# Kernel optimization log

Measured on AMD Instinct MI355X. Metric: run time of the kernel, lower is better.

Reference implementation:

```python
import jax, jax.numpy as jnp
import numpy as np

B, N, K, D, A, V = 2, 32768, 16, 256, 64, 64


def setup_inputs() -> dict:
    key = jax.random.key(0)
    ks = jax.random.split(key, 20)
    r = lambda i, shape: jax.random.normal(ks[i], shape, jnp.float32) * 0.02
    return dict(
        x=jax.random.normal(ks[0], (B, N, D), jnp.float32),
        knn_idx=jax.random.randint(ks[1], (N, K), 0, N),
        knn_rel_pos=jax.random.normal(ks[2], (N, K, 3), jnp.float32),
        g1=jnp.ones((D,), jnp.float32), b1=jnp.zeros((D,), jnp.float32),
        g2=jnp.ones((D,), jnp.float32), b2=jnp.zeros((D,), jnp.float32),
        Wq=r(3, (D, A)), bq=jnp.zeros((A,), jnp.float32),
        Wk=r(4, (D, A)), bk=jnp.zeros((A,), jnp.float32),
        Wv=r(5, (D, V)), bv=jnp.zeros((V,), jnp.float32),
        Wo=r(6, (V, D)), bo=jnp.zeros((D,), jnp.float32),
        Wpa1=r(7, (3, A)), bpa1=jnp.zeros((A,), jnp.float32),
        Wpa2=r(8, (A, A)), bpa2=jnp.zeros((A,), jnp.float32),
        Wpv1=r(9, (3, V)), bpv1=jnp.zeros((V,), jnp.float32),
        Wpv2=r(10, (V, V)), bpv2=jnp.zeros((V,), jnp.float32),
        Ws1=r(11, (A, A)), bs1=jnp.zeros((A,), jnp.float32),
        Ws2=r(12, (A, 1)), bs2=jnp.zeros((1,), jnp.float32),
        Wf1=r(13, (D, 2 * D)), bf1=jnpp if False else jnp.zeros((2 * D,), jnp.float32),
        Wf2=r(14, (2 * D, D)), bf2=jnp.zeros((D,), jnp.float32),
    )


def _ln(t, g, b):
    m = t.mean(-1, keepdims=True)
    var = ((t - m) ** 2).mean(-1, keepdims=True)
    return (t - m) * jax.lax.rsqrt(var + 1e-5) * g + b


def reference(x, knn_idx, knn_rel_pos, g1, b1, g2, b2,
              Wq, bq, Wk, bk, Wv, bv, Wo, bo,
              Wpa1, bpa1, Wpa2, bpa2, Wpv1, bpv1, Wpv2, bpv2,
              Ws1, bs1, Ws2, bs2, Wf1, bf1, Wf2, bf2):
    scale = jnp.sqrt(jnp.float32(A))
    h = _ln(x, g1, b1)                       # [B,N,D]
    q = h @ Wq + bq                          # [B,N,A]
    k_all = h @ Wk + bk                      # [B,N,A]
    v_all = h @ Wv + bv                      # [B,N,V]
    kn = k_all[:, knn_idx]                   # gather -> [B,N,K,A]
    vn = v_all[:, knn_idx]                   # [B,N,K,V]
    ra = jax.nn.relu(knn_rel_pos @ Wpa1 + bpa1) @ Wpa2 + bpa2  # [N,K,A]
    rv = jax.nn.relu(knn_rel_pos @ Wpv1 + bpv1) @ Wpv2 + bpv2  # [N,K,V]
    t = jnp.tanh(q[:, :, None, :] - kn + ra[None])             # [B,N,K,A]
    score = (jax.nn.relu(t @ Ws1 + bs1) @ Ws2 + bs2)[..., 0]   # [B,N,K]
    attn = jax.nn.softmax(score / scale, axis=2)
    ctx = jnp.einsum('bnk,bnkv->bnv', attn, vn + rv[None])     # [B,N,V]
    x = x + ctx @ Wo + bo
    h2 = _ln(x, g2, b2)
    x = x + (jax.nn.gelu(h2 @ Wf1 + bf1, approximate=False) @ Wf2 + bf2)
    return x
```

## Files before the change

kernel.cpp:

```cpp
#include <hip/hip_runtime.h>
#include <hip/hip_bf16.h>
#include <math.h>

#define BB 2
#define NN 32768
#define KK 16
#define DD 256
#define AA 64
#define VV 64

typedef __attribute__((ext_vector_type(8))) short bf16x8;
typedef __attribute__((ext_vector_type(4))) float f32x4;
typedef __attribute__((ext_vector_type(4))) unsigned short u16x4;

__device__ __forceinline__ ushort f2bf(float v) {
  __hip_bfloat16 b = __float2bfloat16(v);
  ushort u; __builtin_memcpy(&u, &b, 2);
  return u;
}

__device__ __forceinline__ void astore(ushort* A, int row, int col, float v) {
  int off = (row * 128 + col * 2) ^ ((row & 7) << 4);
  *reinterpret_cast<ushort*>(reinterpret_cast<char*>(A) + off) = f2bf(v);
}
__device__ __forceinline__ void zstore8(ushort* A, int row, int chunk) {
  int off = (row * 128 + chunk * 8) ^ ((row & 7) << 4);
  *reinterpret_cast<unsigned long long*>(reinterpret_cast<char*>(A) + off) = 0ULL;
}
__device__ __forceinline__ bf16x8 afrag(const ushort* A, int rowbase, int lane, int ks) {
  int row = rowbase + (lane & 15), g = lane >> 4;
  int off = (row * 128 + ks * 64 + g * 16) ^ ((row & 7) << 4);
  return *reinterpret_cast<const bf16x8*>(reinterpret_cast<const char*>(A) + off);
}
__device__ __forceinline__ bf16x8 loadfrag(const ushort* p, int fi, int lane) {
  return *reinterpret_cast<const bf16x8*>(&p[((size_t)fi * 64 + lane) * 8]);
}

__global__ __launch_bounds__(256) void k_prep(
    const float* __restrict__ Wq, const float* __restrict__ Wk, const float* __restrict__ Wv,
    const float* __restrict__ Wf1, const float* __restrict__ Wf2,
    const float* __restrict__ Wpa2, const float* __restrict__ Wpv2,
    const float* __restrict__ Ws1, const float* __restrict__ Wo,
    ushort* __restrict__ pQKV, ushort* __restrict__ pWf1, ushort* __restrict__ pWf2,
    ushort* __restrict__ pS, ushort* __restrict__ pWo) {
  int tid = blockIdx.x * 256 + threadIdx.x;
  int lane = tid & 63, g = lane >> 4, c16 = lane & 15;
  bf16x8 f;
  if (tid < 6144) {
    int fi = tid >> 6; int ks = fi / 12, nt = fi % 12;
    int col = nt * 16 + c16;
    const float* W = (col < 64) ? Wq : (col < 128) ? Wk : Wv;
    int c = col & 63;
#pragma unroll
    for (int e = 0; e < 8; e++) f[e] = (short)f2bf(W[(ks * 32 + g * 8 + e) * 64 + c]);
    *reinterpret_cast<bf16x8*>(&pQKV[(size_t)tid * 8]) = f;
  } else if (tid < 22528) {
    int t2 = tid - 6144; int fi = t2 >> 6; int ks = fi >> 5, nt = fi & 31;
    int col = nt * 16 + c16;
#pragma unroll
    for (int e = 0; e < 8; e++) f[e] = (short)f2bf(Wf1[(ks * 32 + g * 8 + e) * 512 + col]);
    *reinterpret_cast<bf16x8*>(&pWf1[(size_t)t2 * 8]) = f;
  } else if (tid < 38912) {
    int t3 = tid - 22528; int fi = t3 >> 6; int ks = fi >> 4, nt = fi & 15;
    int col = nt * 16 + c16;
#pragma unroll
    for (int e = 0; e < 8; e++) f[e] = (short)f2bf(Wf2[(ks * 32 + g * 8 + e) * 256 + col]);
    *reinterpret_cast<bf16x8*>(&pWf2[(size_t)t3 * 8]) = f;
  } else if (tid < 40448) {
    int t4 = tid - 38912; int fi = t4 >> 6;
    int mat = fi >> 3, ks = (fi >> 2) & 1, nt = fi & 3;
    const float* W = (mat == 0) ? Wpa2 : (mat == 1) ? Wpv2 : Ws1;
    int col = nt * 16 + c16;
#pragma unroll
    for (int e = 0; e < 8; e++) f[e] = (short)f2bf(W[(ks * 32 + g * 8 + e) * 64 + col]);
    *reinterpret_cast<bf16x8*>(&pS[(size_t)t4 * 8]) = f;
  } else if (tid < 42496) {
    int t5 = tid - 40448; int fi = t5 >> 6; int ks = fi >> 4, nt = fi & 15;
    int col = nt * 16 + c16;
#pragma unroll
    for (int e = 0; e < 8; e++) f[e] = (short)f2bf(Wo[(ks * 32 + g * 8 + e) * 256 + col]);
    *reinterpret_cast<bf16x8*>(&pWo[(size_t)t5 * 8]) = f;
  }
}

__global__ __launch_bounds__(256) void k_qkv(
    const float* __restrict__ x, const float* __restrict__ g1, const float* __restrict__ b1,
    const ushort* __restrict__ pW,
    const float* __restrict__ bq, const float* __restrict__ bk, const float* __restrict__ bv,
    float* __restrict__ qo, float* __restrict__ ko, float* __restrict__ vo) {
  __shared__ __align__(16) ushort hs[32 * 256];
  int t = threadIdx.x, lane = t & 63, w = t >> 6;
  size_t row0 = (size_t)blockIdx.x * 32;

  {
    const float4 gv = *reinterpret_cast<const float4*>(&g1[lane * 4]);
    const float4 bvv = *reinterpret_cast<const float4*>(&b1[lane * 4]);
#pragma unroll
    for (int r8 = 0; r8 < 8; r8++) {
      int r = w * 8 + r8;
      const float4 xv = *reinterpret_cast<const float4*>(&x[(row0 + r) * DD + lane * 4]);
      float s = xv.x + xv.y + xv.z + xv.w;
      float s2 = xv.x * xv.x + xv.y * xv.y + xv.z * xv.z + xv.w * xv.w;
      for (int o = 32; o > 0; o >>= 1) { s += __shfl_down(s, o, 64); s2 += __shfl_down(s2, o, 64); }
      s = __shfl(s, 0, 64); s2 = __shfl(s2, 0, 64);
      float m = s * (1.f / DD), rs = rsqrtf(s2 * (1.f / DD) - m * m + 1e-5f);
      u16x4 hv;
      hv[0] = f2bf((xv.x - m) * rs * gv.x + bvv.x);
      hv[1] = f2bf((xv.y - m) * rs * gv.y + bvv.y);
      hv[2] = f2bf((xv.z - m) * rs * gv.z + bvv.z);
      hv[3] = f2bf((xv.w - m) * rs * gv.w + bvv.w);
      int off = (r * 512 + lane * 8) ^ ((r & 7) << 4);
      *reinterpret_cast<u16x4*>(reinterpret_cast<char*>(hs) + off) = hv;
    }
  }
  __syncthreads();

  f32x4 acc[2][3] = {};
  for (int ks = 0; ks < 8; ks++) {
    int rowa = lane & 15, g = lane >> 4;
    bf16x8 a0 = *reinterpret_cast<const bf16x8*>(reinterpret_cast<const char*>(hs) +
                 ((rowa * 512 + ks * 64 + g * 16) ^ ((rowa & 7) << 4)));
    int rowb = rowa + 16;
    bf16x8 a1 = *reinterpret_cast<const bf16x8*>(reinterpret_cast<const char*>(hs) +
                 ((rowb * 512 + ks * 64 + g * 16) ^ ((rowb & 7) << 4)));
#pragma unroll
    for (int j = 0; j < 3; j++) {
      int fi = ks * 12 + w * 3 + j;
      bf16x8 bw = *reinterpret_cast<const bf16x8*>(&pW[((size_t)fi * 64 + lane) * 8]);
      acc[0][j] = __builtin_amdgcn_mfma_f32_16x16x32_bf16(a0, bw, acc[0][j], 0, 0, 0);
      acc[1][j] = __builtin_amdgcn_mfma_f32_16x16x32_bf16(a1, bw, acc[1][j], 0, 0, 0);
    }
  }

#pragma unroll
  for (int j = 0; j < 3; j++) {
    int ntg = w * 3 + j;
    int buf = ntg >> 2;
    float* out = (buf == 0) ? qo : (buf == 1) ? ko : vo;
    const float* bias = (buf == 0) ? bq : (buf == 1) ? bk : bv;
    int col = (ntg & 3) * 16 + (lane & 15);
    float bb = bias[col];
#pragma unroll
    for (int mt = 0; mt < 2; mt++)
#pragma unroll
      for (int r = 0; r < 4; r++) {
        int row = mt * 16 + (lane >> 4) * 4 + r;
        out[(row0 + row) * 64 + col] = acc[mt][j][r] + bb;
      }
  }
}

__global__ __launch_bounds__(256) void k_attn(
    const float* __restrict__ x, const float* __restrict__ relpos, const int* __restrict__ knn,
    const float* __restrict__ qg, const float* __restrict__ kg, const float* __restrict__ vg,
    const float* __restrict__ Wpa1, const float* __restrict__ bpa1, const float* __restrict__ bpa2,
    const float* __restrict__ Wpv1, const float* __restrict__ bpv1, const float* __restrict__ bpv2,
    const ushort* __restrict__ pS, const float* __restrict__ bs1,
    const float* __restrict__ Ws2, const float* __restrict__ bs2,
    const ushort* __restrict__ pWo, const float* __restrict__ bo,
    float* __restrict__ xmid) {
  int n0 = blockIdx.x * 2;
  int t = threadIdx.x, lane = t & 63, w = t >> 6;
  int g = lane >> 4, c16 = lane & 15;

  __shared__ __align__(16) ushort A0[64 * 64];
  __shared__ float ra_ls[32][64];
  __shared__ float rv_ls[32][64];
  __shared__ __align__(16) ushort ctile[16 * 64];
  __shared__ float qv[4][64];
  __shared__ float scp[64][4];
  __shared__ float attn_s[64];
  __shared__ float rp_s[2][48];
  __shared__ int idx_s[2][16];

  if (t < 32) idx_s[t >> 4][t & 15] = knn[(n0 + (t >> 4)) * KK + (t & 15)];
  if (t >= 64 && t < 160) {
    int i = t - 64;
    rp_s[i / 48][i % 48] = relpos[(size_t)n0 * 48 + i];
  }
  if (t >= 160 && t < 160 + 192) {
    int i = t - 160;
    zstore8(ctile, 4 + (i >> 4), i & 15);
  }
  qv[w][lane] = qg[((size_t)(w & 1) * NN + n0 + (w >> 1)) * AA + lane];
  __syncthreads();

  {
    const float* W1 = (w < 2) ? Wpa1 : Wpv1;
    const float* bb1 = (w < 2) ? bpa1 : bpv1;
    float wa0 = W1[lane], wa1 = W1[64 + lane], wa2 = W1[128 + lane], ba = bb1[lane];
    int pt = w & 1;
#pragma unroll
    for (int j = 0; j < 16; j++) {
      float r0 = rp_s[pt][j * 3], r1 = rp_s[pt][j * 3 + 1], r2 = rp_s[pt][j * 3 + 2];
      float v = fmaxf(ba + r0 * wa0 + r1 * wa1 + r2 * wa2, 0.f);
      astore(A0, w * 16 + j, lane, v);
    }
  }
  __syncthreads();

  {
    bf16x8 bwa0 = loadfrag(pS, 0 + 0 + w, lane);
    bf16x8 bwa1 = loadfrag(pS, 0 + 4 + w, lane);
    bf16x8 bwv0 = loadfrag(pS, 8 + 0 + w, lane);
    bf16x8 bwv1 = loadfrag(pS, 8 + 4 + w, lane);
    int col = w * 16 + c16;
    float ba2 = bpa2[col], bv2 = bpv2[col];
#pragma unroll
    for (int mt = 0; mt < 2; mt++) {
      bf16x8 a0 = afrag(A0, mt * 16, lane, 0), a1 = afrag(A0, mt * 16, lane, 1);
      f32x4 acc = {0.f, 0.f, 0.f, 0.f};
      acc = __builtin_amdgcn_mfma_f32_16x16x32_bf16(a0, bwa0, acc, 0, 0, 0);
      acc = __builtin_amdgcn_mfma_f32_16x16x32_bf16(a1, bwa1, acc, 0, 0, 0);
#pragma unroll
      for (int r = 0; r < 4; r++) ra_ls[mt * 16 + g * 4 + r][col] = acc[r] + ba2;
      bf16x8 v0 = afrag(A0, 32 + mt * 16, lane, 0), v1 = afrag(A0, 32 + mt * 16, lane, 1);
      f32x4 accv = {0.f, 0.f, 0.f, 0.f};
      accv = __builtin_amdgcn_mfma_f32_16x16x32_bf16(v0, bwv0, accv, 0, 0, 0);
      accv = __builtin_amdgcn_mfma_f32_16x16x32_bf16(v1, bwv1, accv, 0, 0, 0);
#pragma unroll
      for (int r = 0; r < 4; r++) rv_ls[mt * 16 + g * 4 + r][col] = accv[r] + bv2;
    }
  }
  __syncthreads();

  {
    int pt = w >> 1, b = w & 1;
    float qq = qv[w][lane];
#pragma unroll
    for (int k = 0; k < 16; k++) {
      float kvv = kg[((size_t)b * NN + idx_s[pt][k]) * AA + lane];
      float xx = qq - kvv + ra_ls[pt * 16 + k][lane];
      float ex = __expf(2.f * xx);
      float tv = 1.f - 2.f * __builtin_amdgcn_rcpf(ex + 1.f);
      astore(A0, w * 16 + k, lane, tv);
    }
  }
  __syncthreads();

  {
    bf16x8 fsA = loadfrag(pS, 16 + 0 + w, lane);
    bf16x8 fsB = loadfrag(pS, 16 + 4 + w, lane);
    int col = w * 16 + c16;
    float bsc = bs1[col], wsc = Ws2[col];
    f32x4 pp[4];
#pragma unroll
    for (int mt = 0; mt < 4; mt++) {
      bf16x8 a0 = afrag(A0, mt * 16, lane, 0), a1 = afrag(A0, mt * 16, lane, 1);
      f32x4 acc = {0.f, 0.f, 0.f, 0.f};
      acc = __builtin_amdgcn_mfma_f32_16x16x32_bf16(a0, fsA, acc, 0, 0, 0);
      acc = __builtin_amdgcn_mfma_f32_16x16x32_bf16(a1, fsB, acc, 0, 0, 0);
#pragma unroll
      for (int r = 0; r < 4; r++) acc[r] = fmaxf(acc[r] + bsc, 0.f) * wsc;
      pp[mt] = acc;
    }
#pragma unroll
    for (int o = 1; o < 16; o <<= 1)
#pragma unroll
      for (int mt = 0; mt < 4; mt++)
#pragma unroll
        for (int r = 0; r < 4; r++) pp[mt][r] += __shfl_xor(pp[mt][r], o, 64);
    if (c16 == 0)
#pragma unroll
      for (int mt = 0; mt < 4; mt++)
#pragma unroll
        for (int r = 0; r < 4; r++) scp[mt * 16 + g * 4 + r][w] = pp[mt][r];
  }
  __syncthreads();

  if (t < 64) {
    float4 s4 = *reinterpret_cast<const float4*>(&scp[t][0]);
    float sc = (s4.x + s4.y + s4.z + s4.w + bs2[0]) * 0.125f;
    float mx = sc;
#pragma unroll
    for (int o = 8; o > 0; o >>= 1) mx = fmaxf(mx, __shfl_xor(mx, o, 64));
    float e = __expf(sc - mx);
    float ss = e;
#pragma unroll
    for (int o = 8; o > 0; o >>= 1) ss += __shfl_xor(ss, o, 64);
    attn_s[t] = e / ss;
  }
  __syncthreads();

  {
    int pt = w >> 1, b = w & 1;
    float acc = 0.f;
#pragma unroll
    for (int k = 0; k < 16; k++) {
      float vn = vg[((size_t)b * NN + idx_s[pt][k]) * VV + lane] + rv_ls[pt * 16 + k][lane];
      acc += attn_s[w * 16 + k] * vn;
    }
    astore(ctile, w, lane, acc);
  }
  __syncthreads();

  {
    bf16x8 a0 = afrag(ctile, 0, lane, 0), a1 = afrag(ctile, 0, lane, 1);
    f32x4 acc[4];
#pragma unroll
    for (int j = 0; j < 4; j++) {
      bf16x8 b0 = loadfrag(pWo, 0 + w * 4 + j, lane);
      bf16x8 b1 = loadfrag(pWo, 16 + w * 4 + j, lane);
      f32x4 a = {0.f, 0.f, 0.f, 0.f};
      a = __builtin_amdgcn_mfma_f32_16x16x32_bf16(a0, b0, a, 0, 0, 0);
      a = __builtin_amdgcn_mfma_f32_16x16x32_bf16(a1, b1, a, 0, 0, 0);
      acc[j] = a;
    }
    if (g == 0) {
#pragma unroll
      for (int j = 0; j < 4; j++) {
        int col = w * 64 + j * 16 + c16;
        float bb = bo[col];
#pragma unroll
        for (int r = 0; r < 4; r++) {
          int pt = r >> 1, b = r & 1;
          size_t addr = ((size_t)b * NN + n0 + pt) * DD + col;
          xmid[addr] = x[addr] + acc[j][r] + bb;
        }
      }
    }
  }
}

__global__ __launch_bounds__(256) void k_ffn(
    const float* __restrict__ xmid, const float* __restrict__ g2, const float* __restrict__ b2,
    const ushort* __restrict__ pWf1, const float* __restrict__ bf1,
    const ushort* __restrict__ pWf2, const float* __restrict__ bf2,
    float* __restrict__ out) {
  __shared__ __align__(16) ushort hs[32 * 256];
  __shared__ __align__(16) ushort ys[32 * 512];
  int t = threadIdx.x, lane = t & 63, w = t >> 6;
  size_t row0 = (size_t)blockIdx.x * 32;

  {
    const float4 gv = *reinterpret_cast<const float4*>(&g2[lane * 4]);
    const float4 bvv = *reinterpret_cast<const float4*>(&b2[lane * 4]);
#pragma unroll
    for (int r8 = 0; r8 < 8; r8++) {
      int r = w * 8 + r8;
      const float4 xv = *reinterpret_cast<const float4*>(&xmid[(row0 + r) * DD + lane * 4]);
      float s = xv.x + xv.y + xv.z + xv.w;
      float s2 = xv.x * xv.x + xv.y * xv.y + xv.z * xv.z + xv.w * xv.w;
      for (int o = 32; o > 0; o >>= 1) { s += __shfl_down(s, o, 64); s2 += __shfl_down(s2, o, 64); }
      s = __shfl(s, 0, 64); s2 = __shfl(s2, 0, 64);
      float m = s * (1.f / DD), rs = rsqrtf(s2 * (1.f / DD) - m * m + 1e-5f);
      u16x4 hv;
      hv[0] = f2bf((xv.x - m) * rs * gv.x + bvv.x);
      hv[1] = f2bf((xv.y - m) * rs * gv.y + bvv.y);
      hv[2] = f2bf((xv.z - m) * rs * gv.z + bvv.z);
      hv[3] = f2bf((xv.w - m) * rs * gv.w + bvv.w);
      int off = (r * 512 + lane * 8) ^ ((r & 7) << 4);
      *reinterpret_cast<u16x4*>(reinterpret_cast<char*>(hs) + off) = hv;
    }
  }
  __syncthreads();

  f32x4 acc1[2][8] = {};
  for (int ks = 0; ks < 8; ks++) {
    int rowa = lane & 15, g = lane >> 4;
    bf16x8 a0 = *reinterpret_cast<const bf16x8*>(reinterpret_cast<const char*>(hs) +
                 ((rowa * 512 + ks * 64 + g * 16) ^ ((rowa & 7) << 4)));
    int rowb = rowa + 16;
    bf16x8 a1 = *reinterpret_cast<const bf16x8*>(reinterpret_cast<const char*>(hs) +
                 ((rowb * 512 + ks * 64 + g * 16) ^ ((rowb & 7) << 4)));
#pragma unroll
    for (int j = 0; j < 8; j++) {
      int fi = ks * 32 + w * 8 + j;
      bf16x8 bw = *reinterpret_cast<const bf16x8*>(&pWf1[((size_t)fi * 64 + lane) * 8]);
      acc1[0][j] = __builtin_amdgcn_mfma_f32_16x16x32_bf16(a0, bw, acc1[0][j], 0, 0, 0);
      acc1[1][j] = __builtin_amdgcn_mfma_f32_16x16x32_bf16(a1, bw, acc1[1][j], 0, 0, 0);
    }
  }

#pragma unroll
  for (int j = 0; j < 8; j++) {
    int col = w * 128 + j * 16 + (lane & 15);
    float bb = bf1[col];
#pragma unroll
    for (int mt = 0; mt < 2; mt++)
#pragma unroll
      for (int r = 0; r < 4; r++) {
        float v = acc1[mt][j][r] + bb;
        v = v * 0.5f * (1.f + erff(v * 0.70710678118654752f));
        int row = mt * 16 + (lane >> 4) * 4 + r;
        int off = (row * 1024 + col * 2) ^ ((row & 7) << 4);
        *reinterpret_cast<ushort*>(reinterpret_cast<char*>(ys) + off) = f2bf(v);
      }
  }
  __syncthreads();

  f32x4 acc2[2][4] = {};
  for (int ks = 0; ks < 16; ks++) {
    int rowa = lane & 15, g = lane >> 4;
    bf16x8 a0 = *reinterpret_cast<const bf16x8*>(reinterpret_cast<const char*>(ys) +
                 ((rowa * 1024 + ks * 64 + g * 16) ^ ((rowa & 7) << 4)));
    int rowb = rowa + 16;
    bf16x8 a1 = *reinterpret_cast<const bf16x8*>(reinterpret_cast<const char*>(ys) +
                 ((rowb * 1024 + ks * 64 + g * 16) ^ ((rowb & 7) << 4)));
#pragma unroll
    for (int j = 0; j < 4; j++) {
      int fi = ks * 16 + w * 4 + j;
      bf16x8 bw = *reinterpret_cast<const bf16x8*>(&pWf2[((size_t)fi * 64 + lane) * 8]);
      acc2[0][j] = __builtin_amdgcn_mfma_f32_16x16x32_bf16(a0, bw, acc2[0][j], 0, 0, 0);
      acc2[1][j] = __builtin_amdgcn_mfma_f32_16x16x32_bf16(a1, bw, acc2[1][j], 0, 0, 0);
    }
  }

#pragma unroll
  for (int j = 0; j < 4; j++) {
    int col = w * 64 + j * 16 + (lane & 15);
    float bb = bf2[col];
#pragma unroll
    for (int mt = 0; mt < 2; mt++)
#pragma unroll
      for (int r = 0; r < 4; r++) {
        int row = mt * 16 + (lane >> 4) * 4 + r;
        size_t idx = (row0 + row) * DD + col;
        out[idx] = xmid[idx] + acc2[mt][j][r] + bb;
      }
  }
}

extern "C" void kernel_launch(void* const* d_in, const int* in_sizes, int n_in,
                              void* d_out, int out_size, void* d_ws, size_t ws_size,
                              hipStream_t stream) {
  const float* x      = (const float*)d_in[0];
  const int*   knn    = (const int*)  d_in[1];
  const float* relpos = (const float*)d_in[2];
  const float* g1     = (const float*)d_in[3];
  const float* b1     = (const float*)d_in[4];
  const float* g2     = (const float*)d_in[5];
  const float* b2     = (const float*)d_in[6];
  const float* Wq     = (const float*)d_in[7];
  const float* bq     = (const float*)d_in[8];
  const float* Wk     = (const float*)d_in[9];
  const float* bk     = (const float*)d_in[10];
  const float* Wv     = (const float*)d_in[11];
  const float* bv     = (const float*)d_in[12];
  const float* Wo     = (const float*)d_in[13];
  const float* bo     = (const float*)d_in[14];
  const float* Wpa1   = (const float*)d_in[15];
  const float* bpa1   = (const float*)d_in[16];
  const float* Wpa2   = (const float*)d_in[17];
  const float* bpa2   = (const float*)d_in[18];
  const float* Wpv1   = (const float*)d_in[19];
  const float* bpv1   = (const float*)d_in[20];
  const float* Wpv2   = (const float*)d_in[21];
  const float* bpv2   = (const float*)d_in[22];
  const float* Ws1    = (const float*)d_in[23];
  const float* bs1    = (const float*)d_in[24];
  const float* Ws2    = (const float*)d_in[25];
  const float* bs2    = (const float*)d_in[26];
  const float* Wf1    = (const float*)d_in[27];
  const float* bf1    = (const float*)d_in[28];
  const float* Wf2    = (const float*)d_in[29];
  const float* bf2    = (const float*)d_in[30];

  float* ws   = (float*)d_ws;
  float* q    = ws;
  float* kk   = q  + (size_t)BB * NN * AA;
  float* vv   = kk + (size_t)BB * NN * AA;
  float* xmid = vv + (size_t)BB * NN * VV;
  ushort* pQKV = (ushort*)(xmid + (size_t)BB * NN * DD);
  ushort* pWf1 = pQKV + 49152;
  ushort* pWf2 = pWf1 + 131072;
  ushort* pS   = pWf2 + 131072;
  ushort* pWo  = pS + 12288;

  k_prep<<<166, 256, 0, stream>>>(Wq, Wk, Wv, Wf1, Wf2, Wpa2, Wpv2, Ws1, Wo,
                                  pQKV, pWf1, pWf2, pS, pWo);
  k_qkv<<<(BB * NN) / 32, 256, 0, stream>>>(x, g1, b1, pQKV, bq, bk, bv, q, kk, vv);
  k_attn<<<NN / 2, 256, 0, stream>>>(x, relpos, knn, q, kk, vv,
                                     Wpa1, bpa1, bpa2, Wpv1, bpv1, bpv2,
                                     pS, bs1, Ws2, bs2, pWo, bo, xmid);
  k_ffn<<<(BB * NN) / 32, 256, 0, stream>>>(xmid, g2, b2, pWf1, bf1, pWf2, bf2, (float*)d_out);
}
```

Baseline: 474.2 us.

## Store q/k/v and positional encodings in bf16 with paired-column processing

q, k and v intermediates are written as bf16 instead of fp32, which halves global traffic for the neighbour gathers in the attention kernel. The ra/rv tables in shared memory become bf16, and the tanh and weighted-sum loops now handle two columns per lane across half the neighbours, with a cross-half shuffle reduction. The score reduction swaps per-lane shuffles for a shared-memory partial buffer summed by 64 threads. Precision drops for q/k/v and the positional terms, and the larger shared-memory footprint may reduce occupancy.

```diff
diff --git a/kernel.cpp b/kernel.cpp
--- a/kernel.cpp
+++ b/kernel.cpp
@@ -18,10 +18,13 @@
   ushort u; __builtin_memcpy(&u, &b, 2);
   return u;
 }
-
-__device__ __forceinline__ void astore(ushort* A, int row, int col, float v) {
-  int off = (row * 128 + col * 2) ^ ((row & 7) << 4);
-  *reinterpret_cast<ushort*>(reinterpret_cast<char*>(A) + off) = f2bf(v);
+__device__ __forceinline__ float bflo(unsigned u) { return __uint_as_float(u << 16); }
+__device__ __forceinline__ float bfhi(unsigned u) { return __uint_as_float(u & 0xffff0000u); }
+
+__device__ __forceinline__ void astore2(ushort* A, int row, int colpair, float lo, float hi) {
+  int off = (row * 128 + colpair * 4) ^ ((row & 7) << 4);
+  unsigned u = ((unsigned)f2bf(hi) << 16) | (unsigned)f2bf(lo);
+  *reinterpret_cast<unsigned*>(reinterpret_cast<char*>(A) + off) = u;
 }
 __device__ __forceinline__ void zstore8(ushort* A, int row, int chunk) {
   int off = (row * 128 + chunk * 8) ^ ((row & 7) << 4);
@@ -87,7 +90,7 @@
     const float* __restrict__ x, const float* __restrict__ g1, const float* __restrict__ b1,
     const ushort* __restrict__ pW,
     const float* __restrict__ bq, const float* __restrict__ bk, const float* __restrict__ bv,
-    float* __restrict__ qo, float* __restrict__ ko, float* __restrict__ vo) {
+    ushort* __restrict__ qo, ushort* __restrict__ ko, ushort* __restrict__ vo) {
   __shared__ __align__(16) ushort hs[32 * 256];
   int t = threadIdx.x, lane = t & 63, w = t >> 6;
   size_t row0 = (size_t)blockIdx.x * 32;
@@ -136,7 +139,7 @@
   for (int j = 0; j < 3; j++) {
     int ntg = w * 3 + j;
     int buf = ntg >> 2;
-    float* out = (buf == 0) ? qo : (buf == 1) ? ko : vo;
+    ushort* out = (buf == 0) ? qo : (buf == 1) ? ko : vo;
     const float* bias = (buf == 0) ? bq : (buf == 1) ? bk : bv;
     int col = (ntg & 3) * 16 + (lane & 15);
     float bb = bias[col];
@@ -145,14 +148,14 @@
 #pragma unroll
       for (int r = 0; r < 4; r++) {
         int row = mt * 16 + (lane >> 4) * 4 + r;
-        out[(row0 + row) * 64 + col] = acc[mt][j][r] + bb;
+        out[(row0 + row) * 64 + col] = f2bf(acc[mt][j][r] + bb);
       }
   }
 }
 
 __global__ __launch_bounds__(256) void k_attn(
     const float* __restrict__ x, const float* __restrict__ relpos, const int* __restrict__ knn,
-    const float* __restrict__ qg, const float* __restrict__ kg, const float* __restrict__ vg,
+    const ushort* __restrict__ qg, const ushort* __restrict__ kg, const ushort* __restrict__ vg,
     const float* __restrict__ Wpa1, const float* __restrict__ bpa1, const float* __restrict__ bpa2,
     const float* __restrict__ Wpv1, const float* __restrict__ bpv1, const float* __restrict__ bpv2,
     const ushort* __restrict__ pS, const float* __restrict__ bs1,
@@ -162,13 +165,14 @@
   int n0 = blockIdx.x * 2;
   int t = threadIdx.x, lane = t & 63, w = t >> 6;
   int g = lane >> 4, c16 = lane & 15;
+  int c2 = lane & 31, kh = lane >> 5;
 
   __shared__ __align__(16) ushort A0[64 * 64];
-  __shared__ float ra_ls[32][64];
-  __shared__ float rv_ls[32][64];
+  __shared__ __align__(16) ushort ra_bs[32][72];
+  __shared__ __align__(16) ushort rv_bs[32][72];
+  __shared__ float hidp[64][68];
   __shared__ __align__(16) ushort ctile[16 * 64];
-  __shared__ float qv[4][64];
-  __shared__ float scp[64][4];
+  __shared__ __align__(8) float qv[4][64];
   __shared__ float attn_s[64];
   __shared__ float rp_s[2][48];
   __shared__ int idx_s[2][16];
@@ -182,28 +186,34 @@
     int i = t - 160;
     zstore8(ctile, 4 + (i >> 4), i & 15);
   }
-  qv[w][lane] = qg[((size_t)(w & 1) * NN + n0 + (w >> 1)) * AA + lane];
+  qv[w][lane] = bflo(qg[((size_t)(w & 1) * NN + n0 + (w >> 1)) * AA + lane]);
   __syncthreads();
 
   {
     const float* W1 = (w < 2) ? Wpa1 : Wpv1;
     const float* bb1 = (w < 2) ? bpa1 : bpv1;
-    float wa0 = W1[lane], wa1 = W1[64 + lane], wa2 = W1[128 + lane], ba = bb1[lane];
     int pt = w & 1;
-#pragma unroll
-    for (int j = 0; j < 16; j++) {
-      float r0 = rp_s[pt][j * 3], r1 = rp_s[pt][j * 3 + 1], r2 = rp_s[pt][j * 3 + 2];
-      float v = fmaxf(ba + r0 * wa0 + r1 * wa1 + r2 * wa2, 0.f);
-      astore(A0, w * 16 + j, lane, v);
-    }
-  }
-  __syncthreads();
-
-  {
-    bf16x8 bwa0 = loadfrag(pS, 0 + 0 + w, lane);
-    bf16x8 bwa1 = loadfrag(pS, 0 + 4 + w, lane);
-    bf16x8 bwv0 = loadfrag(pS, 8 + 0 + w, lane);
-    bf16x8 bwv1 = loadfrag(pS, 8 + 4 + w, lane);
+    int base = (w < 2 ? 0 : 32) + pt * 16;
+    float2 w0 = *reinterpret_cast<const float2*>(&W1[2 * c2]);
+    float2 w1 = *reinterpret_cast<const float2*>(&W1[64 + 2 * c2]);
+    float2 w2 = *reinterpret_cast<const float2*>(&W1[128 + 2 * c2]);
+    float2 bb = *reinterpret_cast<const float2*>(&bb1[2 * c2]);
+#pragma unroll
+    for (int j = 0; j < 8; j++) {
+      int k = kh * 8 + j;
+      float r0 = rp_s[pt][k * 3], r1 = rp_s[pt][k * 3 + 1], r2 = rp_s[pt][k * 3 + 2];
+      float lo = fmaxf(bb.x + r0 * w0.x + r1 * w1.x + r2 * w2.x, 0.f);
+      float hi = fmaxf(bb.y + r0 * w0.y + r1 * w1.y + r2 * w2.y, 0.f);
+      astore2(A0, base + k, c2, lo, hi);
+    }
+  }
+  __syncthreads();
+
+  {
+    bf16x8 bwa0 = loadfrag(pS, 0 + w, lane);
+    bf16x8 bwa1 = loadfrag(pS, 4 + w, lane);
+    bf16x8 bwv0 = loadfrag(pS, 8 + w, lane);
+    bf16x8 bwv1 = loadfrag(pS, 12 + w, lane);
     int col = w * 16 + c16;
     float ba2 = bpa2[col], bv2 = bpv2[col];
 #pragma unroll
@@ -213,37 +223,41 @@
       acc = __builtin_amdgcn_mfma_f32_16x16x32_bf16(a0, bwa0, acc, 0, 0, 0);
       acc = __builtin_amdgcn_mfma_f32_16x16x32_bf16(a1, bwa1, acc, 0, 0, 0);
 #pragma unroll
-      for (int r = 0; r < 4; r++) ra_ls[mt * 16 + g * 4 + r][col] = acc[r] + ba2;
+      for (int r = 0; r < 4; r++) ra_bs[mt * 16 + g * 4 + r][col] = f2bf(acc[r] + ba2);
       bf16x8 v0 = afrag(A0, 32 + mt * 16, lane, 0), v1 = afrag(A0, 32 + mt * 16, lane, 1);
       f32x4 accv = {0.f, 0.f, 0.f, 0.f};
       accv = __builtin_amdgcn_mfma_f32_16x16x32_bf16(v0, bwv0, accv, 0, 0, 0);
       accv = __builtin_amdgcn_mfma_f32_16x16x32_bf16(v1, bwv1, accv, 0, 0, 0);
 #pragma unroll
-      for (int r = 0; r < 4; r++) rv_ls[mt * 16 + g * 4 + r][col] = accv[r] + bv2;
+      for (int r = 0; r < 4; r++) rv_bs[mt * 16 + g * 4 + r][col] = f2bf(accv[r] + bv2);
     }
   }
   __syncthreads();
 
   {
     int pt = w >> 1, b = w & 1;
-    float qq = qv[w][lane];
-#pragma unroll
-    for (int k = 0; k < 16; k++) {
-      float kvv = kg[((size_t)b * NN + idx_s[pt][k]) * AA + lane];
-      float xx = qq - kvv + ra_ls[pt * 16 + k][lane];
-      float ex = __expf(2.f * xx);
-      float tv = 1.f - 2.f * __builtin_amdgcn_rcpf(ex + 1.f);
-      astore(A0, w * 16 + k, lane, tv);
-    }
-  }
-  __syncthreads();
-
-  {
-    bf16x8 fsA = loadfrag(pS, 16 + 0 + w, lane);
-    bf16x8 fsB = loadfrag(pS, 16 + 4 + w, lane);
+    float2 qq = *reinterpret_cast<const float2*>(&qv[w][2 * c2]);
+    size_t bbase = (size_t)b * NN;
+#pragma unroll
+    for (int j = 0; j < 8; j++) {
+      int k = kh * 8 + j;
+      const ushort* krow = kg + (bbase + idx_s[pt][k]) * AA;
+      unsigned ku = *reinterpret_cast<const unsigned*>(&krow[2 * c2]);
+      unsigned ru = *reinterpret_cast<const unsigned*>(&ra_bs[pt * 16 + k][2 * c2]);
+      float x0 = qq.x - bflo(ku) + bflo(ru);
+      float x1 = qq.y - bfhi(ku) + bfhi(ru);
+      float t0 = 1.f - 2.f * __builtin_amdgcn_rcpf(__expf(2.f * x0) + 1.f);
+      float t1 = 1.f - 2.f * __builtin_amdgcn_rcpf(__expf(2.f * x1) + 1.f);
+      astore2(A0, w * 16 + k, c2, t0, t1);
+    }
+  }
+  __syncthreads();
+
+  {
+    bf16x8 fsA = loadfrag(pS, 16 + w, lane);
+    bf16x8 fsB = loadfrag(pS, 20 + w, lane);
     int col = w * 16 + c16;
     float bsc = bs1[col], wsc = Ws2[col];
-    f32x4 pp[4];
 #pragma unroll
     for (int mt = 0; mt < 4; mt++) {
       bf16x8 a0 = afrag(A0, mt * 16, lane, 0), a1 = afrag(A0, mt * 16, lane, 1);
@@ -251,26 +265,20 @@
       acc = __builtin_amdgcn_mfma_f32_16x16x32_bf16(a0, fsA, acc, 0, 0, 0);
       acc = __builtin_amdgcn_mfma_f32_16x16x32_bf16(a1, fsB, acc, 0, 0, 0);
 #pragma unroll
-      for (int r = 0; r < 4; r++) acc[r] = fmaxf(acc[r] + bsc, 0.f) * wsc;
-      pp[mt] = acc;
-    }
-#pragma unroll
-    for (int o = 1; o < 16; o <<= 1)
-#pragma unroll
-      for (int mt = 0; mt < 4; mt++)
-#pragma unroll
-        for (int r = 0; r < 4; r++) pp[mt][r] += __shfl_xor(pp[mt][r], o, 64);
-    if (c16 == 0)
-#pragma unroll
-      for (int mt = 0; mt < 4; mt++)
-#pragma unroll
-        for (int r = 0; r < 4; r++) scp[mt * 16 + g * 4 + r][w] = pp[mt][r];
+      for (int r = 0; r < 4; r++)
+        hidp[mt * 16 + g * 4 + r][col] = fmaxf(acc[r] + bsc, 0.f) * wsc;
+    }
   }
   __syncthreads();
 
   if (t < 64) {
-    float4 s4 = *reinterpret_cast<const float4*>(&scp[t][0]);
-    float sc = (s4.x + s4.y + s4.z + s4.w + bs2[0]) * 0.125f;
+    float s = 0.f;
+#pragma unroll
+    for (int c = 0; c < 16; c++) {
+      float4 v4 = *reinterpret_cast<const float4*>(&hidp[t][c * 4]);
+      s += v4.x + v4.y + v4.z + v4.w;
+    }
+    float sc = (s + bs2[0]) * 0.125f;
     float mx = sc;
 #pragma unroll
     for (int o = 8; o > 0; o >>= 1) mx = fmaxf(mx, __shfl_xor(mx, o, 64));
@@ -284,13 +292,21 @@
 
   {
     int pt = w >> 1, b = w & 1;
-    float acc = 0.f;
-#pragma unroll
-    for (int k = 0; k < 16; k++) {
-      float vn = vg[((size_t)b * NN + idx_s[pt][k]) * VV + lane] + rv_ls[pt * 16 + k][lane];
-      acc += attn_s[w * 16 + k] * vn;
-    }
-    astore(ctile, w, lane, acc);
+    size_t bbase = (size_t)b * NN;
+    float a0 = 0.f, a1 = 0.f;
+#pragma unroll
+    for (int j = 0; j < 8; j++) {
+      int k = kh * 8 + j;
+      const ushort* vrow = vg + (bbase + idx_s[pt][k]) * VV;
+      unsigned vu = *reinterpret_cast<const unsigned*>(&vrow[2 * c2]);
+      unsigned ru = *reinterpret_cast<const unsigned*>(&rv_bs[pt * 16 + k][2 * c2]);
+      float aw = attn_s[w * 16 + k];
+      a0 += aw * (bflo(vu) + bflo(ru));
+      a1 += aw * (bfhi(vu) + bfhi(ru));
+    }
+    a0 += __shfl_xor(a0, 32, 64);
+    a1 += __shfl_xor(a1, 32, 64);
+    if (kh == 0) astore2(ctile, w, c2, a0, a1);
   }
   __syncthreads();
 
@@ -456,11 +472,10 @@
   const float* Wf2    = (const float*)d_in[29];
   const float* bf2    = (const float*)d_in[30];
 
-  float* ws   = (float*)d_ws;
-  float* q    = ws;
-  float* kk   = q  + (size_t)BB * NN * AA;
-  float* vv   = kk + (size_t)BB * NN * AA;
-  float* xmid = vv + (size_t)BB * NN * VV;
+  ushort* qb = (ushort*)d_ws;
+  ushort* kb = qb + (size_t)BB * NN * AA;
+  ushort* vb = kb + (size_t)BB * NN * AA;
+  float* xmid = (float*)(vb + (size_t)BB * NN * VV);
   ushort* pQKV = (ushort*)(xmid + (size_t)BB * NN * DD);
   ushort* pWf1 = pQKV + 49152;
   ushort* pWf2 = pWf1 + 131072;
@@ -469,8 +484,8 @@
 
   k_prep<<<166, 256, 0, stream>>>(Wq, Wk, Wv, Wf1, Wf2, Wpa2, Wpv2, Ws1, Wo,
                                   pQKV, pWf1, pWf2, pS, pWo);
-  k_qkv<<<(BB * NN) / 32, 256, 0, stream>>>(x, g1, b1, pQKV, bq, bk, bv, q, kk, vv);
-  k_attn<<<NN / 2, 256, 0, stream>>>(x, relpos, knn, q, kk, vv,
+  k_qkv<<<(BB * NN) / 32, 256, 0, stream>>>(x, g1, b1, pQKV, bq, bk, bv, qb, kb, vb);
+  k_attn<<<NN / 2, 256, 0, stream>>>(x, relpos, knn, qb, kb, vb,
                                      Wpa1, bpa1, bpa2, Wpv1, bpv1, bpv2,
                                      pS, bs1, Ws2, bs2, pWo, bo, xmid);
   k_ffn<<<(BB * NN) / 32, 256, 0, stream>>>(xmid, g2, b2, pWf1, bf1, pWf2, bf2, (float*)d_out);
```

Measured after the change: 462.4 us. 2.5% less time.
